# Kernel optimization log

Measured on AMD Instinct MI355X. Metric: run time of the kernel, lower is better.

The kernel has to match this reference:

```python
import jax, jax.numpy as jnp
import numpy as np

N_IN = 100_000
N_OUT = 800_000
K = 27          # 3x3x3 kernel offsets
C_IN = 32
C_OUT = 64


def setup_inputs() -> dict:
    key = jax.random.key(0)
    k1, k2, k3, k4, k5, k6 = jax.random.split(key, 6)
    feats = jax.random.normal(k1, (N_IN, C_IN), dtype=jnp.float32)
    weight = jax.random.normal(k2, (K, C_IN, C_OUT), dtype=jnp.float32) * (1.0 / np.sqrt(C_IN * K))
    bias = jax.random.normal(k3, (C_OUT,), dtype=jnp.float32) * 0.01
    # bwd is the inverse sort permutation cached by the paired downsampling conv
    bwd = jax.random.permutation(k4, N_IN).astype(jnp.int64)
    # rulebook: per kernel offset, (input row, output row) pairs
    in_idx = jax.random.randint(k5, (K, N_IN), 0, N_IN, dtype=jnp.int64)
    out_idx = jax.random.randint(k6, (K, N_IN), 0, N_OUT, dtype=jnp.int64)
    return {"feats": feats, "weight": weight, "bias": bias,
            "bwd": bwd, "in_idx": in_idx, "out_idx": out_idx, "n_out": N_OUT}


def reference(feats, weight, bias, bwd, in_idx, out_idx, n_out):
    # 1) recover original feature order (the x.feats[bwd] gather)
    f = feats[bwd]                                   # [N_in, C_in]
    # 2) rulebook gather-GEMM-scatter
    gathered = f[in_idx]                             # [K, P, C_in]
    contrib = jnp.einsum('kpc,kcd->kpd', gathered, weight)  # [K, P, C_out]
    out = jnp.zeros((n_out, C_OUT), dtype=feats.dtype)
    out = out.at[out_idx].add(contrib)               # scatter-add over rulebook
    out = out + bias
    return out
```

## Files before the change

kernel.cpp:

```cpp
#include <hip/hip_runtime.h>

#define C_IN  32
#define C_OUT 64
#define KK    27

using frag_ab = __attribute__((ext_vector_type(8))) short;
using frag_cd = __attribute__((ext_vector_type(4))) float;
using u32x4   = __attribute__((ext_vector_type(4))) unsigned int;

static __device__ inline unsigned short f2bf(float f) {
    unsigned u = __float_as_uint(f);
    return (unsigned short)((u + 0x7fffu + ((u >> 16) & 1u)) >> 16);
}
static __device__ inline unsigned pack2(float a, float b) {
    return (unsigned)f2bf(a) | ((unsigned)f2bf(b) << 16);
}
static __device__ inline float bflo(unsigned u) { return __uint_as_float(u << 16); }
static __device__ inline float bfhi(unsigned u) { return __uint_as_float(u & 0xffff0000u); }

__global__ __launch_bounds__(256) void sic_init_bias(float4* __restrict__ out4,
                                                     const float4* __restrict__ bias4,
                                                     int total4) {
    int idx = blockIdx.x * 256 + threadIdx.x, stride = gridDim.x * 256;
    for (int i = idx; i < total4; i += stride) out4[i] = bias4[i & 15];
}

__global__ __launch_bounds__(256) void sic_scatter(
    const float* __restrict__ feats, const float* __restrict__ weight,
    const int* __restrict__ bwd, const int* __restrict__ in_idx,
    const int* __restrict__ out_idx, float* __restrict__ out, int n_in)
{
    const int k = blockIdx.y, lane = threadIdx.x & 63, wid = threadIdx.x >> 6;
    float w[C_IN];
    const float* wk = weight + k * (C_IN * C_OUT);
#pragma unroll
    for (int i = 0; i < C_IN; ++i) w[i] = wk[i * C_OUT + lane];
    const int waves_total = gridDim.x * 4;
    const long long base = (long long)k * n_in;
    for (int p = blockIdx.x * 4 + wid; p < n_in; p += waves_total) {
        int src = __builtin_amdgcn_readfirstlane(in_idx[base + p]);
        int dst = __builtin_amdgcn_readfirstlane(out_idx[base + p]);
        int row = __builtin_amdgcn_readfirstlane(bwd[src]);
        const float* f = feats + (long long)row * C_IN;
        float acc = 0.0f;
#pragma unroll
        for (int i = 0; i < C_IN; ++i) acc = fmaf(f[i], w[i], acc);
        atomicAdd(out + (long long)dst * C_OUT + lane, acc);
    }
}

__global__ __launch_bounds__(512) void sic_zero(int* __restrict__ p, int n) {
    int i = blockIdx.x * 512 + threadIdx.x, stride = gridDim.x * 512;
    for (; i < n; i += stride) p[i] = 0;
}

__global__ __launch_bounds__(256) void sic_fconv(const float* __restrict__ feats,
                                                 short* __restrict__ featsbf, int n_in) {
    int t = blockIdx.x * 256 + threadIdx.x;
    if (t >= (n_in + 1) * 4) return;
    int row = t >> 2, c8 = (t & 3) * 8;
    uint4 v = {0u, 0u, 0u, 0u};
    if (row < n_in) {
        const float* fp = feats + (size_t)row * C_IN + c8;
        float4 f0 = ((const float4*)fp)[0];
        float4 f1 = ((const float4*)fp)[1];
        v.x = pack2(f0.x, f0.y);
        v.y = pack2(f0.z, f0.w);
        v.z = pack2(f1.x, f1.y);
        v.w = pack2(f1.z, f1.w);
    }
    ((uint4*)featsbf)[t] = v;
}

__global__ __launch_bounds__(256) void sic_wconv(const float* __restrict__ weight,
                                                 short* __restrict__ wfrag) {
    int t = blockIdx.x * 256 + threadIdx.x;
    if (t >= KK * 4 * 64) return;
    int l = t & 63, nb = (t >> 6) & 3, k = t >> 8;
    int g = l >> 4, cl = l & 15;
    const float* wp = weight + (size_t)k * (C_IN * C_OUT) + nb * 16 + cl;
    float r[8];
#pragma unroll
    for (int j = 0; j < 8; ++j) r[j] = wp[(size_t)(g * 8 + j) * C_OUT];
    uint4 v = {pack2(r[0], r[1]), pack2(r[2], r[3]), pack2(r[4], r[5]), pack2(r[6], r[7])};
    ((uint4*)wfrag)[t] = v;
}

__global__ __launch_bounds__(256) void sic_hist3(const int* __restrict__ out_idx_seg,
                                                 int* __restrict__ count,
                                                 int* __restrict__ ord, int pseg) {
    int i = blockIdx.x * 256 + threadIdx.x;
    if (i < pseg) {
        ord[i] = atomicAdd(&count[out_idx_seg[i]], 1);
    }
}

__global__ __launch_bounds__(512) void sic_scanA(const int* __restrict__ in,
                                                 int* __restrict__ outExcl,
                                                 int* __restrict__ sums, int n) {
    __shared__ int sm[512];
    int tid = threadIdx.x;
    int base = blockIdx.x * 2048 + tid * 4;
    int e0 = (base + 0 < n) ? in[base + 0] : 0;
    int e1 = (base + 1 < n) ? in[base + 1] : 0;
    int e2 = (base + 2 < n) ? in[base + 2] : 0;
    int e3 = (base + 3 < n) ? in[base + 3] : 0;
    int s = e0 + e1 + e2 + e3;
    sm[tid] = s;
    __syncthreads();
    for (int off = 1; off < 512; off <<= 1) {
        int t = (tid >= off) ? sm[tid - off] : 0;
        __syncthreads();
        sm[tid] += t;
        __syncthreads();
    }
    int pre = sm[tid] - s;
    if (base + 0 < n) outExcl[base + 0] = pre;
    if (base + 1 < n) outExcl[base + 1] = pre + e0;
    if (base + 2 < n) outExcl[base + 2] = pre + e0 + e1;
    if (base + 3 < n) outExcl[base + 3] = pre + e0 + e1 + e2;
    if (tid == 511) sums[blockIdx.x] = sm[511];
}

__global__ __launch_bounds__(512) void sic_scan_small(int* __restrict__ buf, int n) {
    __shared__ int sm[512];
    int tid = threadIdx.x;
    int e = (tid < n) ? buf[tid] : 0;
    sm[tid] = e;
    __syncthreads();
    for (int off = 1; off < 512; off <<= 1) {
        int t = (tid >= off) ? sm[tid - off] : 0;
        __syncthreads();
        sm[tid] += t;
        __syncthreads();
    }
    if (tid < n) buf[tid] = sm[tid] - e;
}

__global__ __launch_bounds__(512) void sic_addbackA(int* __restrict__ arr,
                                                    const int* __restrict__ sums, int n) {
    int s = sums[blockIdx.x];
    int base = blockIdx.x * 2048 + threadIdx.x * 4;
#pragma unroll
    for (int i = 0; i < 4; ++i)
        if (base + i < n) arr[base + i] += s;
}

__global__ __launch_bounds__(256) void sic_gemm3(
    const int* __restrict__ in_idx,
    const int* __restrict__ out_idx,
    const int* __restrict__ bwd,
    const int* __restrict__ ord,
    const int* __restrict__ startv,
    const short* __restrict__ featsbf,
    const short* __restrict__ wfrag,
    unsigned short* __restrict__ contrib,
    int n_in, int k0, int zrow)
{
    __shared__ unsigned smU[4][16][40];
    const int kk   = k0 + blockIdx.y;
    const int lane = threadIdx.x & 63;
    const int wid  = threadIdx.x >> 6;
    const int g = lane >> 4, cl = lane & 15;

    const frag_ab wa0 = *(const frag_ab*)(wfrag + ((size_t)(kk * 4 + 0) * 64 + lane) * 8);
    const frag_ab wa1 = *(const frag_ab*)(wfrag + ((size_t)(kk * 4 + 1) * 64 + lane) * 8);
    const frag_ab wa2 = *(const frag_ab*)(wfrag + ((size_t)(kk * 4 + 2) * 64 + lane) * 8);
    const frag_ab wa3 = *(const frag_ab*)(wfrag + ((size_t)(kk * 4 + 3) * 64 + lane) * 8);
    const frag_cd zf = {0.f, 0.f, 0.f, 0.f};

    const size_t gk  = (size_t)kk * n_in;
    const size_t sk  = (size_t)blockIdx.y * n_in;
    const int t      = blockIdx.x * 4 + wid;
    const int tbase  = t * 16;
    const int idx    = tbase + cl;
    const bool valid = idx < n_in;

    int row = zrow, pos = 0;
    if (valid) {
        row = bwd[in_idx[gk + idx]];
        int dst = out_idx[gk + idx];
        pos = startv[dst] + ord[sk + idx];
    }

    frag_ab b = *(const frag_ab*)(featsbf + (size_t)row * C_IN + g * 8);
    frag_cd d0 = __builtin_amdgcn_mfma_f32_16x16x32_bf16(wa0, b, zf, 0, 0, 0);
    frag_cd d1 = __builtin_amdgcn_mfma_f32_16x16x32_bf16(wa1, b, zf, 0, 0, 0);
    frag_cd d2 = __builtin_amdgcn_mfma_f32_16x16x32_bf16(wa2, b, zf, 0, 0, 0);
    frag_cd d3 = __builtin_amdgcn_mfma_f32_16x16x32_bf16(wa3, b, zf, 0, 0, 0);

    smU[wid][cl][0  + g * 2 + 0] = pack2(d0[0], d0[1]);
    smU[wid][cl][0  + g * 2 + 1] = pack2(d0[2], d0[3]);
    smU[wid][cl][8  + g * 2 + 0] = pack2(d1[0], d1[1]);
    smU[wid][cl][8  + g * 2 + 1] = pack2(d1[2], d1[3]);
    smU[wid][cl][16 + g * 2 + 0] = pack2(d2[0], d2[1]);
    smU[wid][cl][16 + g * 2 + 1] = pack2(d2[2], d2[3]);
    smU[wid][cl][24 + g * 2 + 0] = pack2(d3[0], d3[1]);
    smU[wid][cl][24 + g * 2 + 1] = pack2(d3[2], d3[3]);
    __syncthreads();

#pragma unroll
    for (int p = 0; p < 2; ++p) {
        int r = (lane >> 3) + p * 8;
        int c = lane & 7;
        u32x4 v = {smU[wid][r][c * 4 + 0], smU[wid][r][c * 4 + 1],
                   smU[wid][r][c * 4 + 2], smU[wid][r][c * 4 + 3]};
        int pos_r = __shfl(pos, r, 64);
        if (tbase + r < n_in) {
            __builtin_nontemporal_store(v,
                (u32x4*)(contrib + (size_t)pos_r * C_OUT + c * 8));
        }
    }
}

__global__ __launch_bounds__(256) void sic_reduce8(
    const unsigned int* __restrict__ contribU,
    const int* __restrict__ startv, const int* __restrict__ count,
    const float* __restrict__ bias, float* __restrict__ out,
    int n_out, int first)
{
    int t = blockIdx.x * 256 + threadIdx.x;
    int dst = t >> 3, c8 = t & 7;
    if (dst >= n_out) return;
    int s = startv[dst], c = count[dst];

    size_t ob = (size_t)dst * C_OUT + c8 * 8;
    float4 a0, a1;
    if (first) {
        a0 = *(const float4*)(bias + c8 * 8);
        a1 = *(const float4*)(bias + c8 * 8 + 4);
    } else {
        a0 = *(const float4*)(out + ob);
        a1 = *(const float4*)(out + ob + 4);
    }
    const u32x4* p = (const u32x4*)(contribU + (size_t)s * 32) + c8;
    for (int j = 0; j < c; j += 4) {
        int cm = c - 1;
        int j1 = (j + 1 < cm) ? j + 1 : cm;
        int j2 = (j + 2 < cm) ? j + 2 : cm;
        int j3 = (j + 3 < cm) ? j + 3 : cm;
        u32x4 v0 = __builtin_nontemporal_load(&p[(size_t)j  * 8]);
        u32x4 v1 = __builtin_nontemporal_load(&p[(size_t)j1 * 8]);
        u32x4 v2 = __builtin_nontemporal_load(&p[(size_t)j2 * 8]);
        u32x4 v3 = __builtin_nontemporal_load(&p[(size_t)j3 * 8]);
        a0.x += bflo(v0.x); a0.y += bfhi(v0.x);
        a0.z += bflo(v0.y); a0.w += bfhi(v0.y);
        a1.x += bflo(v0.z); a1.y += bfhi(v0.z);
        a1.z += bflo(v0.w); a1.w += bfhi(v0.w);
        if (j + 1 < c) {
            a0.x += bflo(v1.x); a0.y += bfhi(v1.x);
            a0.z += bflo(v1.y); a0.w += bfhi(v1.y);
            a1.x += bflo(v1.z); a1.y += bfhi(v1.z);
            a1.z += bflo(v1.w); a1.w += bfhi(v1.w);
        }
        if (j + 2 < c) {
            a0.x += bflo(v2.x); a0.y += bfhi(v2.x);
            a0.z += bflo(v2.y); a0.w += bfhi(v2.y);
            a1.x += bflo(v2.z); a1.y += bfhi(v2.z);
            a1.z += bflo(v2.w); a1.w += bfhi(v2.w);
        }
        if (j + 3 < c) {
            a0.x += bflo(v3.x); a0.y += bfhi(v3.x);
            a0.z += bflo(v3.y); a0.w += bfhi(v3.y);
            a1.x += bflo(v3.z); a1.y += bfhi(v3.z);
            a1.z += bflo(v3.w); a1.w += bfhi(v3.w);
        }
    }
    *(float4*)(out + ob)     = a0;
    *(float4*)(out + ob + 4) = a1;
}

extern "C" void kernel_launch(void* const* d_in, const int* in_sizes, int n_in_cnt,
                              void* d_out, int out_size, void* d_ws, size_t ws_size,
                              hipStream_t stream) {
    const float* feats   = (const float*)d_in[0];
    const float* weight  = (const float*)d_in[1];
    const float* bias    = (const float*)d_in[2];
    const int*   bwd     = (const int*)d_in[3];
    const int*   in_idx  = (const int*)d_in[4];
    const int*   out_idx = (const int*)d_in[5];
    float*       out     = (float*)d_out;

    const int n_in  = in_sizes[0] / C_IN;
    const int n_out = out_size / C_OUT;
    const size_t P  = (size_t)KK * n_in;

    const int NCHA = (n_out + 2047) / 2048;

    const size_t NOUTr   = ((size_t)n_out + 255) & ~(size_t)255;
    const size_t o_cnt   = 0;
    const size_t o_stv   = NOUTr;
    const size_t o_s1    = 2 * NOUTr;
    const size_t o_ord   = (o_s1 + 512 + 255) & ~(size_t)255;
    const size_t o_fbf   = (o_ord + P + 255) & ~(size_t)255;
    const size_t fbf_i   = ((size_t)(n_in + 16) * C_IN * 2 + 3) / 4;
    const size_t o_wfr   = (o_fbf + fbf_i + 255) & ~(size_t)255;
    const size_t wfr_i   = (size_t)KK * 4 * 64 * 8 * 2 / 4;
    const size_t o_ctr   = (o_wfr + wfr_i + 255) & ~(size_t)255;

    const size_t ws_ints = ws_size / 4;
    size_t cap_recs = (ws_ints > o_ctr) ? (ws_ints - o_ctr) / 32 : 0;
    int kseg_max = (int)(cap_recs / (size_t)n_in);
    if (kseg_max > KK) kseg_max = KK;

    if (kseg_max < 1 || NCHA > 512) {
        const int total4 = out_size / 4;
        hipLaunchKernelGGL(sic_init_bias, dim3(2048), dim3(256), 0, stream,
                           (float4*)out, (const float4*)bias, total4);
        hipLaunchKernelGGL(sic_scatter, dim3(160, KK), dim3(256), 0, stream,
                           feats, weight, bwd, in_idx, out_idx, out, n_in);
        return;
    }

    int* ws = (int*)d_ws;
    int* count  = ws + o_cnt;
    int* startv = ws + o_stv;
    int* sums   = ws + o_s1;
    int* ord    = ws + o_ord;
    short* featsbf = (short*)(ws + o_fbf);
    short* wfrag   = (short*)(ws + o_wfr);
    unsigned short* contrib = (unsigned short*)(ws + o_ctr);

    hipLaunchKernelGGL(sic_fconv, dim3(((n_in + 1) * 4 + 255) / 256), dim3(256), 0, stream,
                       feats, featsbf, n_in);
    hipLaunchKernelGGL(sic_wconv, dim3((KK * 4 * 64 + 255) / 256), dim3(256), 0, stream,
                       weight, wfrag);

    const int ntiles  = (n_in + 15) / 16;
    const int gx_gemm = (ntiles + 3) / 4;

    for (int k0 = 0; k0 < KK; k0 += kseg_max) {
        const int kseg = (KK - k0 < kseg_max) ? (KK - k0) : kseg_max;
        const int pseg = kseg * n_in;
        const int gp   = (pseg + 255) / 256;
        const int* oseg = out_idx + (size_t)k0 * n_in;

        hipLaunchKernelGGL(sic_zero, dim3(1024), dim3(512), 0, stream, count, n_out);
        hipLaunchKernelGGL(sic_hist3, dim3(gp), dim3(256), 0, stream,
                           oseg, count, ord, pseg);
        hipLaunchKernelGGL(sic_scanA, dim3(NCHA), dim3(512), 0, stream,
                           count, startv, sums, n_out);
        hipLaunchKernelGGL(sic_scan_small, dim3(1), dim3(512), 0, stream, sums, NCHA);
        hipLaunchKernelGGL(sic_addbackA, dim3(NCHA), dim3(512), 0, stream,
                           startv, sums, n_out);
        hipLaunchKernelGGL(sic_gemm3, dim3(gx_gemm, kseg), dim3(256), 0, stream,
                           in_idx, out_idx, bwd, ord, startv,
                           featsbf, wfrag, contrib, n_in, k0, n_in);
        hipLaunchKernelGGL(sic_reduce8, dim3((n_out * 8 + 255) / 256), dim3(256), 0, stream,
                           (const unsigned int*)contrib, startv, count, bias, out,
                           n_out, (k0 == 0) ? 1 : 0);
    }
}
```

Measured before the change: 354.4 us.

## Merge conversion and scan kernels, use memset, process two tiles per wave

Merges the feature and weight bf16 conversion kernels into one launch. Replaces the small scan plus add-back pair with a kernel where each block rescans the chunk sums itself. Replaces the zeroing kernel with hipMemsetAsync. The gather-GEMM kernel now handles two 16-row tiles per wave to expose more memory-level parallelism, at the cost of higher register and LDS use per block and half as many blocks.

```diff
diff --git a/kernel.cpp b/kernel.cpp
--- a/kernel.cpp
+++ b/kernel.cpp
@@ -49,41 +49,39 @@
     }
 }
 
-__global__ __launch_bounds__(512) void sic_zero(int* __restrict__ p, int n) {
-    int i = blockIdx.x * 512 + threadIdx.x, stride = gridDim.x * 512;
-    for (; i < n; i += stride) p[i] = 0;
-}
-
-__global__ __launch_bounds__(256) void sic_fconv(const float* __restrict__ feats,
-                                                 short* __restrict__ featsbf, int n_in) {
-    int t = blockIdx.x * 256 + threadIdx.x;
-    if (t >= (n_in + 1) * 4) return;
-    int row = t >> 2, c8 = (t & 3) * 8;
-    uint4 v = {0u, 0u, 0u, 0u};
-    if (row < n_in) {
-        const float* fp = feats + (size_t)row * C_IN + c8;
-        float4 f0 = ((const float4*)fp)[0];
-        float4 f1 = ((const float4*)fp)[1];
-        v.x = pack2(f0.x, f0.y);
-        v.y = pack2(f0.z, f0.w);
-        v.z = pack2(f1.x, f1.y);
-        v.w = pack2(f1.z, f1.w);
-    }
-    ((uint4*)featsbf)[t] = v;
-}
-
-__global__ __launch_bounds__(256) void sic_wconv(const float* __restrict__ weight,
-                                                 short* __restrict__ wfrag) {
-    int t = blockIdx.x * 256 + threadIdx.x;
-    if (t >= KK * 4 * 64) return;
-    int l = t & 63, nb = (t >> 6) & 3, k = t >> 8;
-    int g = l >> 4, cl = l & 15;
-    const float* wp = weight + (size_t)k * (C_IN * C_OUT) + nb * 16 + cl;
-    float r[8];
-#pragma unroll
-    for (int j = 0; j < 8; ++j) r[j] = wp[(size_t)(g * 8 + j) * C_OUT];
-    uint4 v = {pack2(r[0], r[1]), pack2(r[2], r[3]), pack2(r[4], r[5]), pack2(r[6], r[7])};
-    ((uint4*)wfrag)[t] = v;
+__global__ __launch_bounds__(256) void sic_fwconv(
+    const float* __restrict__ feats, short* __restrict__ featsbf,
+    const float* __restrict__ weight, short* __restrict__ wfrag,
+    int n_in, int fb_blocks)
+{
+    if ((int)blockIdx.x < fb_blocks) {
+        int t = blockIdx.x * 256 + threadIdx.x;
+        if (t >= (n_in + 1) * 4) return;
+        int row = t >> 2, c8 = (t & 3) * 8;
+        uint4 v = {0u, 0u, 0u, 0u};
+        if (row < n_in) {
+            const float* fp = feats + (size_t)row * C_IN + c8;
+            float4 f0 = ((const float4*)fp)[0];
+            float4 f1 = ((const float4*)fp)[1];
+            v.x = pack2(f0.x, f0.y);
+            v.y = pack2(f0.z, f0.w);
+            v.z = pack2(f1.x, f1.y);
+            v.w = pack2(f1.z, f1.w);
+        }
+        ((uint4*)featsbf)[t] = v;
+    } else {
+        int t = (blockIdx.x - fb_blocks) * 256 + threadIdx.x;
+        if (t >= KK * 4 * 64) return;
+        int l = t & 63, nb = (t >> 6) & 3, k = t >> 8;
+        int g = l >> 4, cl = l & 15;
+        const float* wp = weight + (size_t)k * (C_IN * C_OUT) + nb * 16 + cl;
+        float r[8];
+#pragma unroll
+        for (int j = 0; j < 8; ++j) r[j] = wp[(size_t)(g * 8 + j) * C_OUT];
+        uint4 v = {pack2(r[0], r[1]), pack2(r[2], r[3]),
+                   pack2(r[4], r[5]), pack2(r[6], r[7])};
+        ((uint4*)wfrag)[t] = v;
+    }
 }
 
 __global__ __launch_bounds__(256) void sic_hist3(const int* __restrict__ out_idx_seg,
@@ -122,10 +120,12 @@
     if (tid == 511) sums[blockIdx.x] = sm[511];
 }
 
-__global__ __launch_bounds__(512) void sic_scan_small(int* __restrict__ buf, int n) {
+__global__ __launch_bounds__(512) void sic_scanB(int* __restrict__ startv,
+                                                 const int* __restrict__ sums,
+                                                 int nch, int n) {
     __shared__ int sm[512];
     int tid = threadIdx.x;
-    int e = (tid < n) ? buf[tid] : 0;
+    int e = (tid < nch) ? sums[tid] : 0;
     sm[tid] = e;
     __syncthreads();
     for (int off = 1; off < 512; off <<= 1) {
@@ -134,19 +134,14 @@
         sm[tid] += t;
         __syncthreads();
     }
-    if (tid < n) buf[tid] = sm[tid] - e;
-}
-
-__global__ __launch_bounds__(512) void sic_addbackA(int* __restrict__ arr,
-                                                    const int* __restrict__ sums, int n) {
-    int s = sums[blockIdx.x];
-    int base = blockIdx.x * 2048 + threadIdx.x * 4;
+    int add = (blockIdx.x > 0) ? sm[blockIdx.x - 1] : 0;
+    int base = blockIdx.x * 2048 + tid * 4;
 #pragma unroll
     for (int i = 0; i < 4; ++i)
-        if (base + i < n) arr[base + i] += s;
-}
-
-__global__ __launch_bounds__(256) void sic_gemm3(
+        if (base + i < n) startv[base + i] += add;
+}
+
+__global__ __launch_bounds__(256) void sic_gemm3b(
     const int* __restrict__ in_idx,
     const int* __restrict__ out_idx,
     const int* __restrict__ bwd,
@@ -157,7 +152,7 @@
     unsigned short* __restrict__ contrib,
     int n_in, int k0, int zrow)
 {
-    __shared__ unsigned smU[4][16][40];
+    __shared__ unsigned smU[4][2][16][40];
     const int kk   = k0 + blockIdx.y;
     const int lane = threadIdx.x & 63;
     const int wid  = threadIdx.x >> 6;
@@ -171,44 +166,69 @@
 
     const size_t gk  = (size_t)kk * n_in;
     const size_t sk  = (size_t)blockIdx.y * n_in;
-    const int t      = blockIdx.x * 4 + wid;
-    const int tbase  = t * 16;
-    const int idx    = tbase + cl;
-    const bool valid = idx < n_in;
-
-    int row = zrow, pos = 0;
-    if (valid) {
-        row = bwd[in_idx[gk + idx]];
-        int dst = out_idx[gk + idx];
-        pos = startv[dst] + ord[sk + idx];
-    }
-
-    frag_ab b = *(const frag_ab*)(featsbf + (size_t)row * C_IN + g * 8);
-    frag_cd d0 = __builtin_amdgcn_mfma_f32_16x16x32_bf16(wa0, b, zf, 0, 0, 0);
-    frag_cd d1 = __builtin_amdgcn_mfma_f32_16x16x32_bf16(wa1, b, zf, 0, 0, 0);
-    frag_cd d2 = __builtin_amdgcn_mfma_f32_16x16x32_bf16(wa2, b, zf, 0, 0, 0);
-    frag_cd d3 = __builtin_amdgcn_mfma_f32_16x16x32_bf16(wa3, b, zf, 0, 0, 0);
-
-    smU[wid][cl][0  + g * 2 + 0] = pack2(d0[0], d0[1]);
-    smU[wid][cl][0  + g * 2 + 1] = pack2(d0[2], d0[3]);
-    smU[wid][cl][8  + g * 2 + 0] = pack2(d1[0], d1[1]);
-    smU[wid][cl][8  + g * 2 + 1] = pack2(d1[2], d1[3]);
-    smU[wid][cl][16 + g * 2 + 0] = pack2(d2[0], d2[1]);
-    smU[wid][cl][16 + g * 2 + 1] = pack2(d2[2], d2[3]);
-    smU[wid][cl][24 + g * 2 + 0] = pack2(d3[0], d3[1]);
-    smU[wid][cl][24 + g * 2 + 1] = pack2(d3[2], d3[3]);
+    const int tp     = blockIdx.x * 4 + wid;
+    const int t0     = tp * 2, t1 = t0 + 1;
+    const int idx0   = t0 * 16 + cl;
+    const int idx1   = t1 * 16 + cl;
+    const bool v0 = idx0 < n_in, v1 = idx1 < n_in;
+
+    int row0 = zrow, pos0 = 0, row1 = zrow, pos1 = 0;
+    if (v0) {
+        row0 = bwd[in_idx[gk + idx0]];
+        pos0 = startv[out_idx[gk + idx0]] + ord[sk + idx0];
+    }
+    if (v1) {
+        row1 = bwd[in_idx[gk + idx1]];
+        pos1 = startv[out_idx[gk + idx1]] + ord[sk + idx1];
+    }
+
+    frag_ab b0 = *(const frag_ab*)(featsbf + (size_t)row0 * C_IN + g * 8);
+    frag_ab b1 = *(const frag_ab*)(featsbf + (size_t)row1 * C_IN + g * 8);
+
+    frag_cd d00 = __builtin_amdgcn_mfma_f32_16x16x32_bf16(wa0, b0, zf, 0, 0, 0);
+    frag_cd d01 = __builtin_amdgcn_mfma_f32_16x16x32_bf16(wa1, b0, zf, 0, 0, 0);
+    frag_cd d02 = __builtin_amdgcn_mfma_f32_16x16x32_bf16(wa2, b0, zf, 0, 0, 0);
+    frag_cd d03 = __builtin_amdgcn_mfma_f32_16x16x32_bf16(wa3, b0, zf, 0, 0, 0);
+    frag_cd d10 = __builtin_amdgcn_mfma_f32_16x16x32_bf16(wa0, b1, zf, 0, 0, 0);
+    frag_cd d11 = __builtin_amdgcn_mfma_f32_16x16x32_bf16(wa1, b1, zf, 0, 0, 0);
+    frag_cd d12 = __builtin_amdgcn_mfma_f32_16x16x32_bf16(wa2, b1, zf, 0, 0, 0);
+    frag_cd d13 = __builtin_amdgcn_mfma_f32_16x16x32_bf16(wa3, b1, zf, 0, 0, 0);
+
+    smU[wid][0][cl][0  + g * 2 + 0] = pack2(d00[0], d00[1]);
+    smU[wid][0][cl][0  + g * 2 + 1] = pack2(d00[2], d00[3]);
+    smU[wid][0][cl][8  + g * 2 + 0] = pack2(d01[0], d01[1]);
+    smU[wid][0][cl][8  + g * 2 + 1] = pack2(d01[2], d01[3]);
+    smU[wid][0][cl][16 + g * 2 + 0] = pack2(d02[0], d02[1]);
+    smU[wid][0][cl][16 + g * 2 + 1] = pack2(d02[2], d02[3]);
+    smU[wid][0][cl][24 + g * 2 + 0] = pack2(d03[0], d03[1]);
+    smU[wid][0][cl][24 + g * 2 + 1] = pack2(d03[2], d03[3]);
+    smU[wid][1][cl][0  + g * 2 + 0] = pack2(d10[0], d10[1]);
+    smU[wid][1][cl][0  + g * 2 + 1] = pack2(d10[2], d10[3]);
+    smU[wid][1][cl][8  + g * 2 + 0] = pack2(d11[0], d11[1]);
+    smU[wid][1][cl][8  + g * 2 + 1] = pack2(d11[2], d11[3]);
+    smU[wid][1][cl][16 + g * 2 + 0] = pack2(d12[0], d12[1]);
+    smU[wid][1][cl][16 + g * 2 + 1] = pack2(d12[2], d12[3]);
+    smU[wid][1][cl][24 + g * 2 + 0] = pack2(d13[0], d13[1]);
+    smU[wid][1][cl][24 + g * 2 + 1] = pack2(d13[2], d13[3]);
     __syncthreads();
 
 #pragma unroll
     for (int p = 0; p < 2; ++p) {
         int r = (lane >> 3) + p * 8;
         int c = lane & 7;
-        u32x4 v = {smU[wid][r][c * 4 + 0], smU[wid][r][c * 4 + 1],
-                   smU[wid][r][c * 4 + 2], smU[wid][r][c * 4 + 3]};
-        int pos_r = __shfl(pos, r, 64);
-        if (tbase + r < n_in) {
-            __builtin_nontemporal_store(v,
-                (u32x4*)(contrib + (size_t)pos_r * C_OUT + c * 8));
+        u32x4 va = {smU[wid][0][r][c * 4 + 0], smU[wid][0][r][c * 4 + 1],
+                    smU[wid][0][r][c * 4 + 2], smU[wid][0][r][c * 4 + 3]};
+        int pa = __shfl(pos0, r, 64);
+        if (t0 * 16 + r < n_in) {
+            __builtin_nontemporal_store(va,
+                (u32x4*)(contrib + (size_t)pa * C_OUT + c * 8));
+        }
+        u32x4 vb = {smU[wid][1][r][c * 4 + 0], smU[wid][1][r][c * 4 + 1],
+                    smU[wid][1][r][c * 4 + 2], smU[wid][1][r][c * 4 + 3]};
+        int pb = __shfl(pos1, r, 64);
+        if (t1 * 16 + r < n_in) {
+            __builtin_nontemporal_store(vb,
+                (u32x4*)(contrib + (size_t)pb * C_OUT + c * 8));
         }
     }
 }
@@ -321,13 +341,13 @@
     short* wfrag   = (short*)(ws + o_wfr);
     unsigned short* contrib = (unsigned short*)(ws + o_ctr);
 
-    hipLaunchKernelGGL(sic_fconv, dim3(((n_in + 1) * 4 + 255) / 256), dim3(256), 0, stream,
-                       feats, featsbf, n_in);
-    hipLaunchKernelGGL(sic_wconv, dim3((KK * 4 * 64 + 255) / 256), dim3(256), 0, stream,
-                       weight, wfrag);
+    const int fb_blocks = ((n_in + 1) * 4 + 255) / 256;
+    const int wb_blocks = (KK * 4 * 64 + 255) / 256;
+    hipLaunchKernelGGL(sic_fwconv, dim3(fb_blocks + wb_blocks), dim3(256), 0, stream,
+                       feats, featsbf, weight, wfrag, n_in, fb_blocks);
 
     const int ntiles  = (n_in + 15) / 16;
-    const int gx_gemm = (ntiles + 3) / 4;
+    const int gx_gemm = (ntiles + 7) / 8;
 
     for (int k0 = 0; k0 < KK; k0 += kseg_max) {
         const int kseg = (KK - k0 < kseg_max) ? (KK - k0) : kseg_max;
@@ -335,15 +355,14 @@
         const int gp   = (pseg + 255) / 256;
         const int* oseg = out_idx + (size_t)k0 * n_in;
 
-        hipLaunchKernelGGL(sic_zero, dim3(1024), dim3(512), 0, stream, count, n_out);
+        hipMemsetAsync(count, 0, (size_t)n_out * sizeof(int), stream);
         hipLaunchKernelGGL(sic_hist3, dim3(gp), dim3(256), 0, stream,
                            oseg, count, ord, pseg);
         hipLaunchKernelGGL(sic_scanA, dim3(NCHA), dim3(512), 0, stream,
                            count, startv, sums, n_out);
-        hipLaunchKernelGGL(sic_scan_small, dim3(1), dim3(512), 0, stream, sums, NCHA);
-        hipLaunchKernelGGL(sic_addbackA, dim3(NCHA), dim3(512), 0, stream,
-                           startv, sums, n_out);
-        hipLaunchKernelGGL(sic_gemm3, dim3(gx_gemm, kseg), dim3(256), 0, stream,
+        hipLaunchKernelGGL(sic_scanB, dim3(NCHA), dim3(512), 0, stream,
+                           startv, sums, NCHA, n_out);
+        hipLaunchKernelGGL(sic_gemm3b, dim3(gx_gemm, kseg), dim3(256), 0, stream,
                            in_idx, out_idx, bwd, ord, startv,
                            featsbf, wfrag, contrib, n_in, k0, n_in);
         hipLaunchKernelGGL(sic_reduce8, dim3((n_out * 8 + 255) / 256), dim3(256), 0, stream,
```

Result: faster. 346.8 us (-2.1%).
